# Performance work log

Hardware: AMD Instinct MI355X
Metric: run time of the kernel (lower is better)

The kernel has to match this reference:

```python
import jax, jax.numpy as jnp
import numpy as np
from jax.scipy.special import logsumexp

B, T, S, V = 64, 1024, 512, 1024


def setup_inputs() -> dict:
    key = jax.random.key(0)
    k_obs, k_emis, k_trans, k_prior = jax.random.split(key, 4)
    observations = jax.random.randint(k_obs, (B, T), 0, V, dtype=jnp.int32)
    emission_table = jax.random.normal(k_emis, (V, S), dtype=jnp.float32)
    transitions = jax.random.normal(k_trans, (S, S), dtype=jnp.float32)
    prior = jax.random.normal(k_prior, (S,), dtype=jnp.float32)
    return {
        "observations": observations,
        "emission_table": emission_table,
        "transitions": transitions,
        "prior": prior,
    }


def reference(observations, emission_table, transitions, prior):
    # alpha_0[b, s] = emission_logits(obs_0)[b, s] + prior[s]
    alpha0 = emission_table[observations[:, 0]] + prior  # [B, S]

    def step(alpha, obs_t):
        # new_alpha[b, j] = emis[b, j] + logsumexp_i(alpha[b, i] + trans[i, j])
        e = emission_table[obs_t]  # [B, S]
        a = e + logsumexp(alpha[:, :, None] + transitions[None, :, :], axis=1)
        return a, None

    # scan over time steps 1..T-1; xs is [T-1, B]
    alpha, _ = jax.lax.scan(step, alpha0, observations[:, 1:].T)
    return logsumexp(alpha, axis=1)  # [B]
```

## Files before the change

kernel.cpp:

```cpp
#include <hip/hip_runtime.h>


constexpr int Bn = 64, Tn = 1024, Sn = 512;
#define L2E 1.44269504f
#define AS 592

typedef int v4i __attribute__((ext_vector_type(4)));

#if __has_builtin(__builtin_amdgcn_update_dpp)
template <int CTRL>
__device__ __forceinline__ float dpp_fmax(float x) {
    int s = __builtin_bit_cast(int, x);
    int d = __builtin_amdgcn_update_dpp(s, s, CTRL, 0xf, 0xf, false);
    return fmaxf(x, __builtin_bit_cast(float, d));
}
__device__ __forceinline__ float wave_max64(float x) {
    x = dpp_fmax<0x121>(x);
    x = dpp_fmax<0x122>(x);
    x = dpp_fmax<0x124>(x);
    x = dpp_fmax<0x128>(x);
    x = dpp_fmax<0x142>(x);
    x = dpp_fmax<0x143>(x);
    return __builtin_bit_cast(float,
        __builtin_amdgcn_readlane(__builtin_bit_cast(int, x), 63));
}
#else
__device__ __forceinline__ float wave_max64(float x) {
    #pragma unroll
    for (int off = 32; off; off >>= 1) x = fmaxf(x, __shfl_xor(x, off, 64));
    return x;
}
#endif

__device__ __forceinline__ int bfrag_addr(int i, int c) {
    return ((((c >> 4) * 8 + (i >> 6)) * 64) + ((i >> 4) & 3) * 16 + (c & 15)) * 16
           + (i & 15);
}

__global__ __launch_bounds__(256) void prep_rows(
    const float* __restrict__ trans, unsigned char* __restrict__ EqB,
    float* __restrict__ rowmax)
{
    const int i = blockIdx.x;
    const int j = threadIdx.x;
    const int lane = j & 63, wv = j >> 6;
    float t0 = trans[i * Sn + j];
    float t1 = trans[i * Sn + j + 256];
    float m = fmaxf(t0, t1);
    #pragma unroll
    for (int off = 32; off; off >>= 1) m = fmaxf(m, __shfl_xor(m, off, 64));
    __shared__ float rm[4];
    if (lane == 0) rm[wv] = m;
    __syncthreads();
    m = fmaxf(fmaxf(rm[0], rm[1]), fmaxf(rm[2], rm[3]));
    if (j == 0) rowmax[i] = m;
    int q0 = __float2int_rn(127.f * __expf(t0 - m));
    int q1 = __float2int_rn(127.f * __expf(t1 - m));
    EqB[bfrag_addr(i, j)] = (unsigned char)q0;
    EqB[bfrag_addr(i, j + 256)] = (unsigned char)q1;
}

__global__ __launch_bounds__(512) void prep_scale(
    const float* __restrict__ rowmax, float* __restrict__ lr,
    float* __restrict__ Cp)
{
    const int i = threadIdx.x;
    const int lane = i & 63, wv = i >> 6;
    float m = rowmax[i];
    float rm = m;
    #pragma unroll
    for (int off = 32; off; off >>= 1) rm = fmaxf(rm, __shfl_xor(rm, off, 64));
    __shared__ float red[8];
    if (lane == 0) red[wv] = rm;
    __syncthreads();
    float RM = red[0];
    #pragma unroll
    for (int w = 1; w < 8; ++w) RM = fmaxf(RM, red[w]);
    lr[i] = (m - RM) * L2E + 6.98868469f;
    if (i == 0) *Cp = RM - 9.68837417f;
}

__global__ __launch_bounds__(512, 2) void hmm_fwd(
    const int* __restrict__ obs,
    const float* __restrict__ emis,
    const float* __restrict__ prior,
    const v4i* __restrict__ EqB4,
    const float* __restrict__ lr,
    const float* __restrict__ Cp,
    float* __restrict__ out)
{
    const int b = blockIdx.x;
    const int tid = threadIdx.x;
    const int lane = tid & 63, wv = tid >> 6;
    const int m16 = lane & 15, q = lane >> 4;

    __shared__ int obs_s[Tn];
    __shared__ __align__(16) unsigned char PqA[16 * AS];
    __shared__ int Cid[Sn];
    __shared__ __align__(32) float redm[2][8];
    __shared__ float reds[8];

    obs_s[tid] = obs[b * Tn + tid];
    obs_s[tid + 512] = obs[b * Tn + 512 + tid];

    v4i Bf[4][8];
    #pragma unroll
    for (int tau = 0; tau < 4; ++tau)
        #pragma unroll
        for (int kap = 0; kap < 8; ++kap)
            Bf[tau][kap] = EqB4[((wv * 4 + tau) * 8 + kap) * 64 + lane];

    const float lr_t = lr[tid];
    const float C = *Cp;

    __syncthreads();

    float a = emis[obs_s[0] * Sn + tid] + prior[tid];
    float e_next = emis[obs_s[1] * Sn + tid];

    const v4i* Aled = (const v4i*)(PqA + m16 * AS + q * 16);

    for (int t = 1; t < Tn; ++t) {
        const int pb = t & 1;

        float mw = wave_max64(a);
        if (lane == 0) redm[pb][wv] = mw;
        __syncthreads();
        const float4* rmv = (const float4*)redm[pb];
        float4 r0 = rmv[0], r1 = rmv[1];
        float m = fmaxf(fmaxf(fmaxf(r0.x, r0.y), fmaxf(r0.z, r0.w)),
                        fmaxf(fmaxf(r1.x, r1.y), fmaxf(r1.z, r1.w)));

        int gi = __float2int_rn(exp2f(fmaf(a - m, L2E, lr_t)));
        PqA[tid] = (unsigned char)gi;
        __syncthreads();

        float e_cur = e_next;
        if (t < Tn - 1) e_next = emis[obs_s[t + 1] * Sn + tid];

        v4i Af[8];
        #pragma unroll
        for (int kap = 0; kap < 8; ++kap) Af[kap] = Aled[kap * 4];

        v4i acc[4];
        #pragma unroll
        for (int tau = 0; tau < 4; ++tau) {
            v4i z = {0, 0, 0, 0};
            #pragma unroll
            for (int kap = 0; kap < 8; ++kap)
                z = __builtin_amdgcn_mfma_i32_16x16x64_i8(Af[kap], Bf[tau][kap],
                                                          z, 0, 0, 0);
            acc[tau] = z;
        }

        if (lane < 16) {
            #pragma unroll
            for (int tau = 0; tau < 4; ++tau)
                Cid[wv * 64 + tau * 16 + lane] = acc[tau].x;
        }
        __syncthreads();
        int idot = Cid[tid];

        a = e_cur + m + C + __logf((float)idot);
    }

    float m = a;
    #pragma unroll
    for (int off = 32; off; off >>= 1) m = fmaxf(m, __shfl_xor(m, off, 64));
    if (lane == 0) redm[0][wv] = m;
    __syncthreads();
    #pragma unroll
    for (int w = 0; w < 8; ++w) m = fmaxf(m, redm[0][w]);

    float s = __expf(a - m);
    #pragma unroll
    for (int off = 32; off; off >>= 1) s += __shfl_xor(s, off, 64);
    if (lane == 0) reds[wv] = s;
    __syncthreads();
    if (tid == 0) {
        float tot = 0.f;
        #pragma unroll
        for (int w = 0; w < 8; ++w) tot += reds[w];
        out[b] = m + __logf(tot);
    }
}

extern "C" void kernel_launch(void* const* d_in, const int* in_sizes, int n_in,
                              void* d_out, int out_size, void* d_ws, size_t ws_size,
                              hipStream_t stream) {
    const int*   obs   = (const int*)d_in[0];
    const float* emis  = (const float*)d_in[1];
    const float* trans = (const float*)d_in[2];
    const float* prior = (const float*)d_in[3];
    float* out = (float*)d_out;

    unsigned char* EqB = (unsigned char*)d_ws;
    float* rowmax = (float*)(EqB + Sn * Sn);
    float* lr     = rowmax + Sn;
    float* Cp     = lr + Sn;

    prep_rows<<<Sn, 256, 0, stream>>>(trans, EqB, rowmax);
    prep_scale<<<1, Sn, 0, stream>>>(rowmax, lr, Cp);
    hmm_fwd<<<Bn, Sn, 0, stream>>>(obs, emis, prior,
                                   (const v4i*)EqB, lr, Cp, out);
}
```

Measured before the change: 1.116 ms.

## Broadcast probability vector into MFMA A rows to drop per-step LDS barrier

The A operand now uses the same 512-byte probability vector for all 16 MFMA rows. That makes every output row identical, so each lane can take its own column result straight from its accumulator. This removes the Cid shared-memory round trip and one __syncthreads per time step. The probability buffer is double-buffered by step parity to avoid write-after-read hazards, and the 8-wave max combine uses a DPP pattern instead of vector loads. The intended gain is lower per-step latency in this serial recurrence. The MFMA still spends its work computing 16 identical rows.

```diff
diff --git a/kernel.cpp b/kernel.cpp
--- a/kernel.cpp
+++ b/kernel.cpp
@@ -3,7 +3,6 @@
 
 constexpr int Bn = 64, Tn = 1024, Sn = 512;
 #define L2E 1.44269504f
-#define AS 592
 
 typedef int v4i __attribute__((ext_vector_type(4)));
 
@@ -24,10 +23,21 @@
     return __builtin_bit_cast(float,
         __builtin_amdgcn_readlane(__builtin_bit_cast(int, x), 63));
 }
+__device__ __forceinline__ float max_of_8_pattern(float x) {
+    x = dpp_fmax<0x121>(x);
+    x = dpp_fmax<0x122>(x);
+    x = dpp_fmax<0x124>(x);
+    return x;
+}
 #else
 __device__ __forceinline__ float wave_max64(float x) {
     #pragma unroll
     for (int off = 32; off; off >>= 1) x = fmaxf(x, __shfl_xor(x, off, 64));
+    return x;
+}
+__device__ __forceinline__ float max_of_8_pattern(float x) {
+    #pragma unroll
+    for (int off = 1; off < 8; off <<= 1) x = fmaxf(x, __shfl_xor(x, off, 64));
     return x;
 }
 #endif
@@ -92,12 +102,11 @@
     const int b = blockIdx.x;
     const int tid = threadIdx.x;
     const int lane = tid & 63, wv = tid >> 6;
-    const int m16 = lane & 15, q = lane >> 4;
+    const int q = lane >> 4;
 
     __shared__ int obs_s[Tn];
-    __shared__ __align__(16) unsigned char PqA[16 * AS];
-    __shared__ int Cid[Sn];
-    __shared__ __align__(32) float redm[2][8];
+    __shared__ __align__(16) unsigned char Pq[2][Sn];
+    __shared__ float redm[2][8];
     __shared__ float reds[8];
 
     obs_s[tid] = obs[b * Tn + tid];
@@ -117,8 +126,6 @@
 
     float a = emis[obs_s[0] * Sn + tid] + prior[tid];
     float e_next = emis[obs_s[1] * Sn + tid];
-
-    const v4i* Aled = (const v4i*)(PqA + m16 * AS + q * 16);
 
     for (int t = 1; t < Tn; ++t) {
         const int pb = t & 1;
@@ -126,21 +133,20 @@
         float mw = wave_max64(a);
         if (lane == 0) redm[pb][wv] = mw;
         __syncthreads();
-        const float4* rmv = (const float4*)redm[pb];
-        float4 r0 = rmv[0], r1 = rmv[1];
-        float m = fmaxf(fmaxf(fmaxf(r0.x, r0.y), fmaxf(r0.z, r0.w)),
-                        fmaxf(fmaxf(r1.x, r1.y), fmaxf(r1.z, r1.w)));
+        float m = max_of_8_pattern(redm[pb][lane & 7]);
 
         int gi = __float2int_rn(exp2f(fmaf(a - m, L2E, lr_t)));
-        PqA[tid] = (unsigned char)gi;
+        Pq[pb][tid] = (unsigned char)gi;
         __syncthreads();
 
         float e_cur = e_next;
         if (t < Tn - 1) e_next = emis[obs_s[t + 1] * Sn + tid];
 
+        const unsigned char* Pbase = Pq[pb] + q * 16;
         v4i Af[8];
         #pragma unroll
-        for (int kap = 0; kap < 8; ++kap) Af[kap] = Aled[kap * 4];
+        for (int kap = 0; kap < 8; ++kap)
+            Af[kap] = *(const v4i*)(Pbase + kap * 64);
 
         v4i acc[4];
         #pragma unroll
@@ -153,13 +159,10 @@
             acc[tau] = z;
         }
 
-        if (lane < 16) {
-            #pragma unroll
-            for (int tau = 0; tau < 4; ++tau)
-                Cid[wv * 64 + tau * 16 + lane] = acc[tau].x;
-        }
-        __syncthreads();
-        int idot = Cid[tid];
+        int idot = (lane < 16) ? acc[0].x
+                 : (lane < 32) ? acc[1].x
+                 : (lane < 48) ? acc[2].x
+                               : acc[3].x;
 
         a = e_cur + m + C + __logf((float)idot);
     }
```

Result: faster. 1.010 ms (-9.5%).
